# Performance work log

Measured on AMD Instinct MI355X. Metric: run time of the kernel, lower is better.

The kernel has to match this reference:

```python
import jax, jax.numpy as jnp
import numpy as np

SCORE_WEIGHT = 0.5
MAX_ITER = 20
PROJ_ITER = 5
RELAX_LR = 0.1
EPS = 1e-8

P, D, T, O, H, W = 256, 256, 2, 24, 240, 432


def setup_inputs() -> dict:
    key = jax.random.key(0)
    k1, k2, k3, k4, k5 = jax.random.split(key, 5)
    proposed_feature = jax.random.normal(k1, (P, D), dtype=jnp.float32)
    proposed_mask = (jax.random.uniform(k2, (P, H, W)) > 0.7).astype(jnp.float32)
    template_feature = jax.random.normal(k3, (T, O, D), dtype=jnp.float32)
    mask_last_occurence = (jax.random.uniform(k4, (O, H, W)) > 0.7).astype(jnp.float32)
    proposal_score = jax.random.uniform(k5, (P,), dtype=jnp.float32)
    return {
        "proposed_feature": proposed_feature,
        "proposed_mask": proposed_mask,
        "template_feature": template_feature,
        "mask_last_occurence": mask_last_occurence,
        "proposal_score": proposal_score,
    }


def relax_matching(C, max_iter=MAX_ITER, proj_iter=PROJ_INNER if False else PROJ_ITER, lr=RELAX_LR):
    """Projected-gradient relaxation of the assignment LP.
    Gradient step on <C, X>, then proj_iter alternating projections onto
    {X >= 0, X <= 1, row sums == 1}. Returns mean of iterates (sum(X_list)/len)."""
    K, N = C.shape
    X0 = jnp.full((K, N), 1.0 / N, dtype=C.dtype)

    def project(X):
        def body(_, X):
            X = jnp.clip(X, 0.0, 1.0)
            X = X / (jnp.sum(X, axis=1, keepdims=True) + EPS)
            return X
        return jax.lax.fori_loop(0, proj_iter, body, X)

    def step(X, _):
        X = project(X - lr * C)
        return X, X

    _, Xs = jax.lax.scan(step, X0, None, length=max_iter)
    return jnp.mean(Xs, axis=0)  # [K, N]


def reference(proposed_feature, proposed_mask, template_feature,
              mask_last_occurence, proposal_score):
    n_prop = proposed_mask.shape[0]
    n_tplt = mask_last_occurence.shape[0]
    h, w = proposed_mask.shape[1], proposed_mask.shape[2]

    # --- feature cosine similarity, averaged over template frames ---
    kf = proposed_feature / (jnp.linalg.norm(proposed_feature, axis=1, keepdims=True) + EPS)
    qf = template_feature / (jnp.linalg.norm(template_feature, axis=2, keepdims=True) + EPS)
    feature_sim = jnp.einsum('tod,pd->op', qf, kf) / template_feature.shape[0]  # [O, P]

    # --- pairwise binary-mask IoU without materializing [O*P, HW] ---
    A = mask_last_occurence.reshape(n_tplt, -1)  # [O, HW] templates
    B = proposed_mask.reshape(n_prop, -1)        # [P, HW] proposals
    inter = A @ B.T                              # [O, P]
    union = A.sum(axis=1)[:, None] + B.sum(axis=1)[None, :] - inter
    iou = inter / (union + EPS)

    sim_matrix = feature_sim * (1.0 - SCORE_WEIGHT) + iou * SCORE_WEIGHT
    # P > O so no padding branch; cost is [O, P]
    cost_matrix = -sim_matrix

    Ridx = relax_matching(cost_matrix)           # averaged iterates, [O, P]
    # training branch (is_test == 0)
    logic_mask = (Ridx > 0.01).astype(Ridx.dtype)
    binX = Ridx * logic_mask

    full_outmask = (binX @ B).reshape(n_tplt, h, w)                 # [O, H, W]
    match_score = jnp.max(jnp.clip(Ridx, 0.0, 1.0) * -cost_matrix, axis=1)  # [O]
    det_score = jnp.sum(proposal_score[None, :] * binX, axis=1)     # [O]
    return (full_outmask, match_score, det_score)
```

## Files before the change

### kernel.cpp

```cpp
#include <hip/hip_runtime.h>

#define HW 103680
#define WORDS 1620
#define NGRP 405
#define NP 256
#define NO 24
#define ND 256
#define EPSF 1e-8f
#define OUTM (NO*HW)
#define NCHUNK 26

typedef unsigned long long u64;
typedef float vfloat4 __attribute__((ext_vector_type(4)));

__device__ __forceinline__ float waveRedSum(float v) {
  v += __int_as_float(__builtin_amdgcn_update_dpp(0, __float_as_int(v), 0x111, 0xf, 0xf, false));
  v += __int_as_float(__builtin_amdgcn_update_dpp(0, __float_as_int(v), 0x112, 0xf, 0xf, false));
  v += __int_as_float(__builtin_amdgcn_update_dpp(0, __float_as_int(v), 0x114, 0xf, 0xf, false));
  v += __int_as_float(__builtin_amdgcn_update_dpp(0, __float_as_int(v), 0x118, 0xf, 0xf, false));
  v += __int_as_float(__builtin_amdgcn_update_dpp(0, __float_as_int(v), 0x142, 0xf, 0xf, false));
  v += __int_as_float(__builtin_amdgcn_update_dpp(0, __float_as_int(v), 0x143, 0xf, 0xf, false));
  return __int_as_float(__builtin_amdgcn_readlane(__float_as_int(v), 63));
}
__device__ __forceinline__ float waveRedMax(float v) {
  int vi = __float_as_int(v);
  v = fmaxf(v, __int_as_float(__builtin_amdgcn_update_dpp(vi, vi, 0x111, 0xf, 0xf, false))); vi = __float_as_int(v);
  v = fmaxf(v, __int_as_float(__builtin_amdgcn_update_dpp(vi, vi, 0x112, 0xf, 0xf, false))); vi = __float_as_int(v);
  v = fmaxf(v, __int_as_float(__builtin_amdgcn_update_dpp(vi, vi, 0x114, 0xf, 0xf, false))); vi = __float_as_int(v);
  v = fmaxf(v, __int_as_float(__builtin_amdgcn_update_dpp(vi, vi, 0x118, 0xf, 0xf, false))); vi = __float_as_int(v);
  v = fmaxf(v, __int_as_float(__builtin_amdgcn_update_dpp(vi, vi, 0x142, 0xf, 0xf, false))); vi = __float_as_int(v);
  v = fmaxf(v, __int_as_float(__builtin_amdgcn_update_dpp(vi, vi, 0x143, 0xf, 0xf, false)));
  return __int_as_float(__builtin_amdgcn_readlane(__float_as_int(v), 63));
}

__global__ __launch_bounds__(256) void pack_kernel(const float* __restrict__ pm,
                                                   const float* __restrict__ ml,
                                                   u64* __restrict__ bbits,
                                                   u64* __restrict__ abits) {
  int W = blockIdx.x * 4 + (threadIdx.x >> 6);
  int lane = threadIdx.x & 63;
  int row = W / NCHUNK;
  int cidx = W - row * NCHUNK;
  const float* rp; u64* bits;
  if (row < NP) { rp = pm + (size_t)row * HW;        bits = bbits + (size_t)row * WORDS; }
  else          { rp = ml + (size_t)(row - NP) * HW; bits = abits + (size_t)(row - NP) * WORDS; }
  int g0 = cidx * 16;
  int k4 = lane >> 2, c = lane & 3;
  u64 myword = 0;
  if (cidx != 25) {
#pragma unroll
    for (int k = 0; k < 16; ++k) {
      vfloat4 v = __builtin_nontemporal_load((const vfloat4*)(rp + (size_t)(g0 + k) * 256 + lane * 4));
      u64 m0 = __ballot(v.x != 0.0f);
      u64 m1 = __ballot(v.y != 0.0f);
      u64 m2 = __ballot(v.z != 0.0f);
      u64 m3 = __ballot(v.w != 0.0f);
      u64 s = (c == 0) ? m0 : (c == 1) ? m1 : (c == 2) ? m2 : m3;
      if (k4 == k) myword = s;
    }
    bits[g0 * 4 + lane] = myword;
  } else {
#pragma unroll
    for (int k = 0; k < 5; ++k) {
      vfloat4 v = __builtin_nontemporal_load((const vfloat4*)(rp + (size_t)(g0 + k) * 256 + lane * 4));
      u64 m0 = __ballot(v.x != 0.0f);
      u64 m1 = __ballot(v.y != 0.0f);
      u64 m2 = __ballot(v.z != 0.0f);
      u64 m3 = __ballot(v.w != 0.0f);
      u64 s = (c == 0) ? m0 : (c == 1) ? m1 : (c == 2) ? m2 : m3;
      if (k4 == k) myword = s;
    }
    if (lane < 20) bits[g0 * 4 + lane] = myword;
  }
}

__global__ __launch_bounds__(256) void interfeat_kernel(const u64* __restrict__ ab,
                                                        const u64* __restrict__ bb,
                                                        const float* __restrict__ pf,
                                                        const float* __restrict__ tf,
                                                        float* __restrict__ C) {
  int wid = (blockIdx.x * 256 + threadIdx.x) >> 6;
  int lane = threadIdx.x & 63;
  int o = wid >> 8, p = wid & 255;
  float4 f = *(const float4*)(pf + p * ND + lane * 4);
  float4 a = *(const float4*)(tf + o * ND + lane * 4);
  float4 b = *(const float4*)(tf + (NO + o) * ND + lane * 4);
  const u64* arl = ab + (size_t)o * WORDS + lane;
  const u64* brl = bb + (size_t)p * WORDS + lane;
  int cnt = 0, ucnt = 0;
#pragma unroll 5
  for (int k = 0; k < 25; ++k) {
    u64 av = arl[k * 64], bv = brl[k * 64];
    cnt  += (int)__popcll(av & bv);
    ucnt += (int)__popcll(av | bv);
  }
  if (lane < WORDS - 1600) {
    u64 av = arl[1600], bv = brl[1600];
    cnt  += (int)__popcll(av & bv);
    ucnt += (int)__popcll(av | bv);
  }
  float inter = waveRedSum((float)cnt);
  float uni   = waveRedSum((float)ucnt);
  float nf = waveRedSum(f.x*f.x + f.y*f.y + f.z*f.z + f.w*f.w);
  float na = waveRedSum(a.x*a.x + a.y*a.y + a.z*a.z + a.w*a.w);
  float nb = waveRedSum(b.x*b.x + b.y*b.y + b.z*b.z + b.w*b.w);
  float d0 = waveRedSum(a.x*f.x + a.y*f.y + a.z*f.z + a.w*f.w);
  float d1 = waveRedSum(b.x*f.x + b.y*f.y + b.z*f.z + b.w*f.w);
  if (lane == 0) {
    float invf = 1.0f / (sqrtf(nf) + EPSF);
    float inva = 1.0f / (sqrtf(na) + EPSF);
    float invb = 1.0f / (sqrtf(nb) + EPSF);
    float fs  = (d0 * inva + d1 * invb) * invf * 0.5f;
    float iou = inter / (uni + EPSF);
    C[wid] = -(fs * 0.5f + iou * 0.5f);
  }
}

__global__ __launch_bounds__(1024) void solmask_kernel(const float* __restrict__ Cm,
                                                       const float* __restrict__ score,
                                                       const u64* __restrict__ bb,
                                                       float* __restrict__ out) {
  int o = blockIdx.x;
  int tid = threadIdx.x, lane = tid & 63, w = tid >> 6;
  __shared__ int   s_nzidx[NP];
  __shared__ float s_nzval[NP];
  __shared__ int   s_nzcnt;

  if (w == 0) {
    float4 c4 = *(const float4*)(Cm + o * NP + lane * 4);
    float C[4] = {c4.x, c4.y, c4.z, c4.w};
    float sim[4], X[4], Xs[4];
#pragma unroll
    for (int j = 0; j < 4; ++j) {
      sim[j] = -C[j];
      X[j] = 1.0f / 256.0f;
      Xs[j] = 0.0f;
    }
    for (int it = 0; it < 20; ++it) {
#pragma unroll
      for (int j = 0; j < 4; ++j) X[j] = X[j] - 0.1f * C[j];
      for (int k = 0; k < 5; ++k) {
#pragma unroll
        for (int j = 0; j < 4; ++j) X[j] = fminf(fmaxf(X[j], 0.0f), 1.0f);
        float s = waveRedSum((X[0] + X[1]) + (X[2] + X[3]));
#pragma unroll
        for (int j = 0; j < 4; ++j) X[j] = X[j] / (s + EPSF);
      }
#pragma unroll
      for (int j = 0; j < 4; ++j) Xs[j] += X[j];
    }
    float R[4], bx[4];
#pragma unroll
    for (int j = 0; j < 4; ++j) {
      R[j] = Xs[j] / 20.0f;
      bx[j] = (R[j] > 0.01f) ? R[j] : 0.0f;
    }
    unsigned long long lt = (1ull << lane) - 1ull;
    int base = 0;
#pragma unroll
    for (int j = 0; j < 4; ++j) {
      unsigned long long m = __ballot(bx[j] != 0.0f);
      if (bx[j] != 0.0f) {
        int pos = base + (int)__popcll(m & lt);
        s_nzidx[pos] = lane * 4 + j;
        s_nzval[pos] = bx[j];
      }
      base += (int)__popcll(m);
    }
    if (lane == 0) s_nzcnt = base;
    float mv = -1e30f;
#pragma unroll
    for (int j = 0; j < 4; ++j)
      mv = fmaxf(mv, fminf(fmaxf(R[j], 0.0f), 1.0f) * sim[j]);
    mv = waveRedMax(mv);
    float4 sc4 = *(const float4*)(score + lane * 4);
    float dv = waveRedSum(((sc4.x * bx[0]) + (sc4.y * bx[1])) + ((sc4.z * bx[2]) + (sc4.w * bx[3])));
    if (lane == 0) { out[OUTM + o] = mv; out[OUTM + NO + o] = dv; }
  }
  __syncthreads();

  int cnt = s_nzcnt;
  for (int g = w; g < NGRP; g += 16) {
    float ax = 0.0f, ay = 0.0f, az = 0.0f, aw = 0.0f;
    for (int t = 0; t < cnt; ++t) {
      int p   = s_nzidx[t];
      float v = s_nzval[t];
      const u64* wp = bb + (size_t)p * WORDS + g * 4;
      u64 m0 = wp[0], m1 = wp[1], m2 = wp[2], m3 = wp[3];
      ax += ((m0 >> lane) & 1ull) ? v : 0.0f;
      ay += ((m1 >> lane) & 1ull) ? v : 0.0f;
      az += ((m2 >> lane) & 1ull) ? v : 0.0f;
      aw += ((m3 >> lane) & 1ull) ? v : 0.0f;
    }
    *(float4*)(out + (size_t)o * HW + g * 256 + lane * 4) = make_float4(ax, ay, az, aw);
  }
}

extern "C" void kernel_launch(void* const* d_in, const int* in_sizes, int n_in,
                              void* d_out, int out_size, void* d_ws, size_t ws_size,
                              hipStream_t stream) {
  const float* pf = (const float*)d_in[0];
  const float* pm = (const float*)d_in[1];
  const float* tf = (const float*)d_in[2];
  const float* ml = (const float*)d_in[3];
  const float* sc = (const float*)d_in[4];
  float* out = (float*)d_out;
  char* ws = (char*)d_ws;

  u64*   bbits = (u64*)(ws);
  u64*   abits = (u64*)(ws + 3317760);
  float* Cm    = (float*)(ws + 3628800);

  hipLaunchKernelGGL(pack_kernel,      dim3(1820), dim3(256),  0, stream, pm, ml, bbits, abits);
  hipLaunchKernelGGL(interfeat_kernel, dim3(1536), dim3(256),  0, stream, abits, bbits, pf, tf, Cm);
  hipLaunchKernelGGL(solmask_kernel,   dim3(24),   dim3(1024), 0, stream, Cm, sc, bbits, out);
}
```

Before: 54.64 us.

## Pack masks by loading only the high byte of each float and use contiguous bit layout

The pack kernel now reads just the most significant byte of each float, relying on the masks being exactly 0.0 or 1.0. Bits are laid out contiguously (bit = pixel within a 64-pixel run) instead of interleaved by float4 component. The output mask writes switch to coalesced scalar stores to match the new bit layout. Byte loads still fetch whole cache lines, so DRAM traffic may barely shrink while the instruction count per pixel grows fourfold, and the sign-byte test is only valid for masks whose nonzero values have a nonzero top byte.

```diff
diff --git a/kernel.cpp b/kernel.cpp
--- a/kernel.cpp
+++ b/kernel.cpp
@@ -11,7 +11,6 @@
 #define NCHUNK 26
 
 typedef unsigned long long u64;
-typedef float vfloat4 __attribute__((ext_vector_type(4)));
 
 __device__ __forceinline__ float waveRedSum(float v) {
   v += __int_as_float(__builtin_amdgcn_update_dpp(0, __float_as_int(v), 0x111, 0xf, 0xf, false));
@@ -41,36 +40,36 @@
   int lane = threadIdx.x & 63;
   int row = W / NCHUNK;
   int cidx = W - row * NCHUNK;
-  const float* rp; u64* bits;
-  if (row < NP) { rp = pm + (size_t)row * HW;        bits = bbits + (size_t)row * WORDS; }
-  else          { rp = ml + (size_t)(row - NP) * HW; bits = abits + (size_t)(row - NP) * WORDS; }
+  const unsigned char* rpb;
+  u64* bits;
+  if (row < NP) { rpb = (const unsigned char*)(pm + (size_t)row * HW);        bits = bbits + (size_t)row * WORDS; }
+  else          { rpb = (const unsigned char*)(ml + (size_t)(row - NP) * HW); bits = abits + (size_t)(row - NP) * WORDS; }
   int g0 = cidx * 16;
-  int k4 = lane >> 2, c = lane & 3;
   u64 myword = 0;
   if (cidx != 25) {
 #pragma unroll
     for (int k = 0; k < 16; ++k) {
-      vfloat4 v = __builtin_nontemporal_load((const vfloat4*)(rp + (size_t)(g0 + k) * 256 + lane * 4));
-      u64 m0 = __ballot(v.x != 0.0f);
-      u64 m1 = __ballot(v.y != 0.0f);
-      u64 m2 = __ballot(v.z != 0.0f);
-      u64 m3 = __ballot(v.w != 0.0f);
-      u64 s = (c == 0) ? m0 : (c == 1) ? m1 : (c == 2) ? m2 : m3;
-      if (k4 == k) myword = s;
+#pragma unroll
+      for (int w2 = 0; w2 < 4; ++w2) {
+        int px = (g0 + k) * 256 + w2 * 64 + lane;
+        unsigned char b = __builtin_nontemporal_load(rpb + (size_t)px * 4 + 3);
+        u64 m = __ballot(b != 0);
+        if (lane == k * 4 + w2) myword = m;
+      }
     }
     bits[g0 * 4 + lane] = myword;
   } else {
 #pragma unroll
     for (int k = 0; k < 5; ++k) {
-      vfloat4 v = __builtin_nontemporal_load((const vfloat4*)(rp + (size_t)(g0 + k) * 256 + lane * 4));
-      u64 m0 = __ballot(v.x != 0.0f);
-      u64 m1 = __ballot(v.y != 0.0f);
-      u64 m2 = __ballot(v.z != 0.0f);
-      u64 m3 = __ballot(v.w != 0.0f);
-      u64 s = (c == 0) ? m0 : (c == 1) ? m1 : (c == 2) ? m2 : m3;
-      if (k4 == k) myword = s;
-    }
-    if (lane < 20) bits[g0 * 4 + lane] = myword;
+#pragma unroll
+      for (int w2 = 0; w2 < 4; ++w2) {
+        int px = (400 + k) * 256 + w2 * 64 + lane;
+        unsigned char b = __builtin_nontemporal_load(rpb + (size_t)px * 4 + 3);
+        u64 m = __ballot(b != 0);
+        if (lane == k * 4 + w2) myword = m;
+      }
+    }
+    if (lane < 20) bits[1600 + lane] = myword;
   }
 }
 
@@ -181,18 +180,22 @@
 
   int cnt = s_nzcnt;
   for (int g = w; g < NGRP; g += 16) {
-    float ax = 0.0f, ay = 0.0f, az = 0.0f, aw = 0.0f;
+    float a0 = 0.0f, a1 = 0.0f, a2 = 0.0f, a3 = 0.0f;
     for (int t = 0; t < cnt; ++t) {
       int p   = s_nzidx[t];
       float v = s_nzval[t];
       const u64* wp = bb + (size_t)p * WORDS + g * 4;
       u64 m0 = wp[0], m1 = wp[1], m2 = wp[2], m3 = wp[3];
-      ax += ((m0 >> lane) & 1ull) ? v : 0.0f;
-      ay += ((m1 >> lane) & 1ull) ? v : 0.0f;
-      az += ((m2 >> lane) & 1ull) ? v : 0.0f;
-      aw += ((m3 >> lane) & 1ull) ? v : 0.0f;
-    }
-    *(float4*)(out + (size_t)o * HW + g * 256 + lane * 4) = make_float4(ax, ay, az, aw);
+      a0 += ((m0 >> lane) & 1ull) ? v : 0.0f;
+      a1 += ((m1 >> lane) & 1ull) ? v : 0.0f;
+      a2 += ((m2 >> lane) & 1ull) ? v : 0.0f;
+      a3 += ((m3 >> lane) & 1ull) ? v : 0.0f;
+    }
+    float* ob = out + (size_t)o * HW + g * 256;
+    ob[lane]       = a0;
+    ob[64 + lane]  = a1;
+    ob[128 + lane] = a2;
+    ob[192 + lane] = a3;
   }
 }
 
```

Result: slower. 63.43 us (+16.1%).
